# Performance work log

Measured on AMD Instinct MI355X. Metric: run time of the kernel, lower is better.

## Reference

```python
import jax, jax.numpy as jnp
import numpy as np

COUNT = 8  # hardcoded 8x8 patch grid in the original module


def setup_inputs() -> dict:
    key = jax.random.key(0)
    kx, = jax.random.split(key, 1)
    x = jax.random.normal(kx, (8, 64, 512, 512), dtype=jnp.float32)
    gamma = jnp.zeros((1,), dtype=jnp.float32)  # nn.Parameter(torch.zeros(1))
    return {"x": x, "gamma": gamma}


def reference(x, gamma):
    B, C, H, W = x.shape
    s = H // COUNT  # stride; original uses height-derived stride for both dims
    # Extract the 8x8 grid of patches without loops:
    # (B,C,H,W) -> (B,C,cnt,s,cnt,s) -> (B,cnt,cnt,C,s,s) -> (B,P,C,s*s)
    p = x.reshape(B, C, COUNT, s, COUNT, s)
    p = p.transpose(0, 2, 4, 1, 3, 5).reshape(B, COUNT * COUNT, C, s * s)
    # channel-channel energy per patch: [B,P,C,C]
    energy = jnp.einsum('bpci,bpdi->bpcd', p, p)
    # DANet trick: max - energy, then softmax over last dim
    energy_new = jnp.max(energy, axis=-1, keepdims=True) - energy
    attention = jax.nn.softmax(energy_new, axis=-1)
    out = jnp.einsum('bpcd,bpdi->bpci', attention, p)
    # reassemble spatial map
    out = out.reshape(B, COUNT, COUNT, C, s, s)
    out = out.transpose(0, 3, 1, 4, 2, 5).reshape(B, C, H, W)
    # NOTE: in the torch code y = x is an alias and x is overwritten in-place,
    # so the final result is gamma * attended + attended.
    return gamma[0] * out + out
```

## Files before the change

### kernel.cpp

```cpp
#include <hip/hip_runtime.h>


#define NW  512
#define HWs 262144

typedef __attribute__((ext_vector_type(4)))  __bf16 bf4;
typedef __attribute__((ext_vector_type(8)))  __bf16 bf8;
typedef __attribute__((ext_vector_type(16))) float  f32x16;

#define MFMA __builtin_amdgcn_mfma_f32_32x32x16_bf16
#define F4E(v,j) ((j)==0?(v).x:(j)==1?(v).y:(j)==2?(v).z:(v).w)

__device__ __forceinline__ void bar_lgkm() {
  asm volatile("s_waitcnt lgkmcnt(0)" ::: "memory");
  __builtin_amdgcn_s_barrier();
}

extern "C" __global__ __launch_bounds__(512)
void k1_gram(const float* __restrict__ x, float* __restrict__ ep,
             __bf16* __restrict__ wsHi) {
  __shared__ char lds[66560];
  char* sHi = lds;
  char* sLo = lds + 32768;
  float* S_lds = (float*)lds;

  const int T   = threadIdx.x;
  const int wv8 = T >> 6;
  const int l   = T & 63;
  const int l31 = l & 31;
  const int hh  = l >> 5;

  const int bid = blockIdx.x;
  const int wh = bid & 1;
  const int hq = (bid >> 1) & 3;
  const int pr = (bid >> 3) & 7;
  const int b  = bid >> 6;

  const int pl = wv8 & 3;
  const int ct = wv8 >> 2;
  const int pc = wh * 4 + pl;
  const int pat  = b * 64 + pr * 8 + pc;
  const int row0 = pr * 64 + hq * 16;

  const float* xb = x + (size_t)b * 64 * HWs + (size_t)row0 * NW + wh * 256 + l * 4;

  f32x16 G0, G1, S0, S1;
#pragma unroll
  for (int i = 0; i < 16; ++i) { G0[i]=0.f; G1[i]=0.f; S0[i]=0.f; S1[i]=0.f; }

  float4 rA[8], rB[8];
#pragma unroll
  for (int j = 0; j < 8; ++j)
    rA[j] = *(const float4*)(xb + (size_t)(wv8 * 8 + j) * HWs);

  for (int r = 0; r < 16; ++r) {
    if (r + 1 < 16) {
#pragma unroll
      for (int j = 0; j < 8; ++j)
        rB[j] = *(const float4*)(xb + (size_t)(wv8 * 8 + j) * HWs + (size_t)(r + 1) * NW);
    }
    bf4 hA[8];
#pragma unroll
    for (int j = 0; j < 8; ++j) {
      const int c = wv8 * 8 + j;
      const float4 v = rA[j];
      bf4 h, lo;
      h[0]=(__bf16)v.x; h[1]=(__bf16)v.y; h[2]=(__bf16)v.z; h[3]=(__bf16)v.w;
      lo[0]=(__bf16)(v.x-(float)h[0]); lo[1]=(__bf16)(v.y-(float)h[1]);
      lo[2]=(__bf16)(v.z-(float)h[2]); lo[3]=(__bf16)(v.w-(float)h[3]);
      hA[j] = h;
      const int off = c * 512 + ((l * 8) ^ ((c & 31) << 4));
      *(bf4*)(sHi + off) = h;
      *(bf4*)(sLo + off) = lo;
    }
#pragma unroll
    for (int k2 = 0; k2 < 4; ++k2) {
      bf8 pk;
#pragma unroll
      for (int jj = 0; jj < 8; ++jj) pk[jj] = hA[jj][k2];
      const int wloc256 = l * 4 + k2;
      const int pl_w = wloc256 >> 6;
      const int w_loc = wloc256 & 63;
      const int pat_w = b * 64 + pr * 8 + wh * 4 + pl_w;
      const int i = (hq * 16 + r) * 64 + w_loc;
      *(bf8*)((char*)wsHi + (size_t)pat_w * 524288 + (size_t)i * 128 + wv8 * 16) = pk;
    }
    bar_lgkm();
#pragma unroll
    for (int ks = 0; ks < 4; ++ks) {
      const int kb = pl * 128 + ks * 32 + hh * 16;
      const int ca = ct * 32 + l31;
      const bf8 a   = *(const bf8*)(sHi + ca * 512 + (kb ^ ((ca & 31) << 4)));
      const bf8 bh0 = *(const bf8*)(sHi + l31 * 512 + (kb ^ ((l31 & 31) << 4)));
      const bf8 bh1 = *(const bf8*)(sHi + (32 + l31) * 512 + (kb ^ (((32 + l31) & 31) << 4)));
      const bf8 bl0 = *(const bf8*)(sLo + l31 * 512 + (kb ^ ((l31 & 31) << 4)));
      const bf8 bl1 = *(const bf8*)(sLo + (32 + l31) * 512 + (kb ^ (((32 + l31) & 31) << 4)));
      G0 = MFMA(a, bh0, G0, 0, 0, 0);
      G1 = MFMA(a, bh1, G1, 0, 0, 0);
      S0 = MFMA(a, bl0, S0, 0, 0, 0);
      S1 = MFMA(a, bl1, S1, 0, 0, 0);
    }
    bar_lgkm();
#pragma unroll
    for (int e = 0; e < 8; ++e) rA[e] = rB[e];
  }

#pragma unroll
  for (int i = 0; i < 16; ++i) {
    const int cr = ct * 32 + (i & 3) + ((i >> 2) << 3) + (hh << 2);
    S_lds[pl * 4160 + cr * 65 + l31]      = S0[i];
    S_lds[pl * 4160 + cr * 65 + 32 + l31] = S1[i];
  }
  bar_lgkm();
  float* epb = ep + ((size_t)(pat * 4 + hq) << 12);
#pragma unroll
  for (int i = 0; i < 16; ++i) {
    const int cr = ct * 32 + (i & 3) + ((i >> 2) << 3) + (hh << 2);
    epb[cr * 64 + l31]      = G0[i] + S0[i] + S_lds[pl * 4160 + l31 * 65 + cr];
    epb[cr * 64 + 32 + l31] = G1[i] + S1[i] + S_lds[pl * 4160 + (32 + l31) * 65 + cr];
  }
}

extern "C" __global__ __launch_bounds__(256)
void k2_softmax(const float* __restrict__ ep, const float* __restrict__ g,
                __bf16* __restrict__ attn) {
  const int pat = blockIdx.x;
  const int w4 = threadIdx.x >> 6, l = threadIdx.x & 63;
  const float gs = 1.0f + g[0];
  const float* e0 = ep + ((size_t)(pat * 4) << 12);
#pragma unroll 1
  for (int cc = 0; cc < 16; ++cc) {
    const int c = w4 * 16 + cc;
    const int o = c * 64 + l;
    const float e = e0[o] + e0[4096 + o] + e0[8192 + o] + e0[12288 + o];
    float mn = e;
#pragma unroll
    for (int off = 32; off; off >>= 1) mn = fminf(mn, __shfl_xor(mn, off));
    const float w = __expf(mn - e);
    float s = w;
#pragma unroll
    for (int off = 32; off; off >>= 1) s += __shfl_xor(s, off);
    attn[(size_t)pat * 4096 + o] = (__bf16)(gs * w / s);
  }
}

extern "C" __global__ __launch_bounds__(512)
void k3_pv(const __bf16* __restrict__ wsHi, const __bf16* __restrict__ attn,
           float* __restrict__ out) {
  __shared__ char lds[65536];
  const int T   = threadIdx.x;
  const int wv8 = T >> 6;
  const int l   = T & 63;
  const int l31 = l & 31;
  const int hh  = l >> 5;

  const int bid = blockIdx.x;
  const int hq = bid & 3;
  const int pr = (bid >> 2) & 7;
  const int b  = bid >> 5;

  const int ii  = T >> 1;
  const int haf = T & 1;

  float4 rS[4], rT[4];
  {
    const size_t src0 = (size_t)(b * 64 + pr * 8) * 524288 + (size_t)(hq * 1024) * 128;
#pragma unroll
    for (int q = 0; q < 4; ++q)
      rS[q] = *(const float4*)((const char*)wsHi + src0 + (size_t)ii * 128 + haf * 64 + q * 16);
  }

  for (int p = 0; p < 8; ++p) {
    const int pat = b * 64 + pr * 8 + p;
    bf8 af[2][4];
#pragma unroll
    for (int mt = 0; mt < 2; ++mt)
#pragma unroll
      for (int ks = 0; ks < 4; ++ks)
        af[mt][ks] = *(const bf8*)(attn + (size_t)pat * 4096 +
                                   (mt * 32 + l31) * 64 + ks * 16 + hh * 8);

    for (int cc = 0; cc < 4; ++cc) {
      const int s = p * 4 + cc;
      char* buf = lds + (s & 1) * 32768;
#pragma unroll
      for (int q = 0; q < 4; ++q) {
        const int off = ii * 128 + (((haf * 64 + q * 16)) ^ ((ii & 7) << 4));
        *(float4*)(buf + off) = rS[q];
      }
      if (s + 1 < 32) {
        const int pn = (s + 1) >> 2, cn = (s + 1) & 3;
        const size_t src = (size_t)(b * 64 + pr * 8 + pn) * 524288 +
                           (size_t)(hq * 1024 + cn * 256) * 128;
#pragma unroll
        for (int q = 0; q < 4; ++q)
          rT[q] = *(const float4*)((const char*)wsHi + src + (size_t)ii * 128 + haf * 64 + q * 16);
      }
      bar_lgkm();

      f32x16 o0, o1;
#pragma unroll
      for (int i = 0; i < 16; ++i) { o0[i] = 0.f; o1[i] = 0.f; }
#pragma unroll
      for (int ks = 0; ks < 4; ++ks) {
        const int irow = wv8 * 32 + l31;
        const bf8 pa = *(const bf8*)(buf + irow * 128 +
                                     (((ks * 32 + hh * 16)) ^ ((irow & 7) << 4)));
        o0 = MFMA(pa, af[0][ks], o0, 0, 0, 0);
        o1 = MFMA(pa, af[1][ks], o1, 0, 0, 0);
      }
      const int i_base = hq * 1024 + cc * 256 + wv8 * 32;
#pragma unroll
      for (int rq = 0; rq < 4; ++rq) {
        const int ig = i_base + rq * 8 + hh * 4;
        const int rl = ig >> 6, wl = ig & 63;
        float* orow = out + (size_t)b * 64 * HWs + (size_t)(pr * 64 + rl) * NW + p * 64 + wl;
        float4 q0; q0.x=o0[rq*4+0]; q0.y=o0[rq*4+1]; q0.z=o0[rq*4+2]; q0.w=o0[rq*4+3];
        *(float4*)(orow + (size_t)l31 * HWs) = q0;
        float4 q1; q1.x=o1[rq*4+0]; q1.y=o1[rq*4+1]; q1.z=o1[rq*4+2]; q1.w=o1[rq*4+3];
        *(float4*)(orow + (size_t)(32 + l31) * HWs) = q1;
      }
      bar_lgkm();
#pragma unroll
      for (int e = 0; e < 4; ++e) rS[e] = rT[e];
    }
  }
}

#define NS1 16
#define NS3 16
__device__ __forceinline__ void fb_load1(const float* g1, int st, float4 (&R)[16]) {
  const float* gp = g1 + (size_t)st * 4 * NW;
#pragma unroll
  for (int rl = 0; rl < 4; ++rl)
#pragma unroll
    for (int j = 0; j < 4; ++j)
      R[rl * 4 + j] = *(const float4*)(gp + (size_t)rl * NW + j * 4);
}
__device__ __forceinline__ void fb_cvtw1(char* wH, char* wL, int q_ld, int swzw,
                                         const float4 (&R)[16]) {
#pragma unroll
  for (int rl = 0; rl < 4; ++rl)
#pragma unroll
    for (int s = 0; s < 2; ++s) {
      const float4 va = R[rl * 4 + s * 2], vb = R[rl * 4 + s * 2 + 1];
      const float f[8] = {va.x, va.y, va.z, va.w, vb.x, vb.y, vb.z, vb.w};
      bf8 h, lo;
#pragma unroll
      for (int e = 0; e < 8; ++e) { h[e] = (__bf16)f[e]; lo[e] = (__bf16)(f[e] - (float)h[e]); }
      const int boff = (rl * 128 + q_ld * 32 + s * 16) ^ swzw;
      *(bf8*)(wH + boff) = h;
      *(bf8*)(wL + boff) = lo;
    }
}
__device__ __forceinline__ void fb_load3(const float* g3, int st, float4 (&R)[16]) {
  const float* gp = g3 + (size_t)st * 4 * NW;
#pragma unroll
  for (int cc = 0; cc < 4; ++cc)
#pragma unroll
    for (int j = 0; j < 4; ++j)
      R[cc * 4 + j] = *(const float4*)(gp + (size_t)cc * HWs + j * 4);
}
__device__ __forceinline__ void fb_cvtw3(char* sT, int cg, int iq, const float4 (&R)[16]) {
#pragma unroll
  for (int w = 0; w < 16; ++w) {
    bf4 q;
#pragma unroll
    for (int cc = 0; cc < 4; ++cc) q[cc] = (__bf16)F4E(R[cc * 4 + (w >> 2)], w & 3);
    const int iloc = iq * 16 + w;
    const int sw = ((iloc & 15) ^ ((iloc >> 4) & 7)) << 4;
    const int boff = (iloc & 127) * 256 + ((((iloc >> 7) << 7) + cg * 8) ^ sw);
    *(bf4*)(sT + boff) = q;
  }
}
extern "C" __global__ __launch_bounds__(256, 2)
void spectralAgg_fallback(const float* __restrict__ x, const float* __restrict__ g,
                          float* __restrict__ out) {
  __shared__ char lds[73728];
  char* sH = lds;
  char* sL = lds + 32768;
  char* sA = lds + 65536;
  const int t = threadIdx.x, wv = t >> 6, l = t & 63, l31 = l & 31, hh = l >> 5;
  const int wg = blockIdx.x, b = wg >> 6, pp = wg & 63, pr = pp >> 3, pcq = pp & 7;
  const size_t pbase = (size_t)b*64*HWs + (size_t)(pr*64)*NW + (size_t)(pcq*64);
  const float* xp = x + pbase;
  float* op = out + pbase;
  const int c_ld = t >> 2, q_ld = t & 3;
  const float* g1 = xp + (size_t)c_ld * HWs + q_ld * 16;
  char* wH = sH + c_ld * 512;
  char* wL = sL + c_ld * 512;
  const int swzw = (c_ld & 31) << 4;
  const int ct = wv >> 1, dt = wv & 1;
  const char* pA  = sH + (size_t)(ct*32+l31)*512;
  const char* pBh = sH + (size_t)(dt*32+l31)*512;
  const char* pBl = sL + (size_t)(dt*32+l31)*512;
  const int swzr = l31 << 4;
  f32x16 accG, accS;
#pragma unroll
  for (int i = 0; i < 16; ++i) { accG[i] = 0.f; accS[i] = 0.f; }
  float4 ra[16], rb[16];
  fb_load1(g1, 0, ra);
  for (int st = 0; st < NS1; ++st) {
    fb_load1(g1, (st + 1 < NS1) ? st + 1 : st, rb);
    fb_cvtw1(wH, wL, q_ld, swzw, ra);
    bar_lgkm();
#pragma unroll
    for (int k0 = 0; k0 < 16; ++k0) {
      const int off = (k0 * 32 + hh * 16) ^ swzr;
      const bf8 a  = *(const bf8*)(pA + off);
      const bf8 bh = *(const bf8*)(pBh + off);
      const bf8 bl = *(const bf8*)(pBl + off);
      accG = MFMA(a, bh, accG, 0, 0, 0);
      accS = MFMA(a, bl, accS, 0, 0, 0);
    }
    bar_lgkm();
#pragma unroll
    for (int e = 0; e < 16; ++e) ra[e] = rb[e];
  }
  float* S_lds = (float*)sL;
  float* E_lds = (float*)sH;
#pragma unroll
  for (int i = 0; i < 16; ++i) {
    const int cr = ct*32 + (i&3) + ((i>>2)<<3) + (hh<<2);
    S_lds[cr*64 + dt*32 + l31] = accS[i];
  }
  bar_lgkm();
#pragma unroll
  for (int i = 0; i < 16; ++i) {
    const int cr = ct*32 + (i&3) + ((i>>2)<<3) + (hh<<2);
    const int d = dt*32 + l31;
    E_lds[cr*64 + d] = accG[i] + accS[i] + S_lds[d*64 + cr];
  }
  bar_lgkm();
  const int cg = t >> 4, iq = t & 15;
  const float* g3 = xp + (size_t)(cg*4)*HWs + (size_t)(iq>>2)*NW + (iq&3)*16;
  fb_load3(g3, 0, ra);
  const float gs = 1.0f + g[0];
#pragma unroll 1
  for (int rr = 0; rr < 16; ++rr) {
    const int c = wv*16 + rr;
    const float e = E_lds[c*64 + l];
    float mn = e;
#pragma unroll
    for (int o = 32; o; o >>= 1) mn = fminf(mn, __shfl_xor(mn, o));
    const float w = __expf(mn - e);
    float s = w;
#pragma unroll
    for (int o = 32; o; o >>= 1) s += __shfl_xor(s, o);
    *(__bf16*)(sA + c*128 + ((l*2) ^ ((c&7)<<4))) = (__bf16)(gs * w / s);
  }
  bar_lgkm();
  bf8 bfr[2][4];
#pragma unroll
  for (int c2 = 0; c2 < 2; ++c2)
#pragma unroll
    for (int k0 = 0; k0 < 4; ++k0)
      bfr[c2][k0] = *(const bf8*)(sA + (size_t)(c2*32+l31)*128 +
                                  ((k0*32 + hh*16) ^ ((l31&7)<<4)));
  for (int st = 0; st < NS3; ++st) {
    fb_load3(g3, (st + 1 < NS3) ? st + 1 : st, rb);
    fb_cvtw3(sH, cg, iq, ra);
    bar_lgkm();
    f32x16 oo0[2], oo1[2];
#pragma unroll
    for (int it = 0; it < 2; ++it)
#pragma unroll
      for (int i = 0; i < 16; ++i) { oo0[it][i] = 0.f; oo1[it][i] = 0.f; }
#pragma unroll
    for (int it = 0; it < 2; ++it) {
      const int i = wv*64 + it*32 + l31;
      const char* base = sH + (size_t)(i & 127) * 256;
      const int hb = (i >> 7) * 128;
      const int sw = ((i & 15) ^ ((i >> 4) & 7)) << 4;
#pragma unroll
      for (int k0 = 0; k0 < 4; ++k0) {
        const bf8 pa = *(const bf8*)(base + ((hb + k0*32 + hh*16) ^ sw));
        oo0[it] = MFMA(pa, bfr[0][k0], oo0[it], 0, 0, 0);
        oo1[it] = MFMA(pa, bfr[1][k0], oo1[it], 0, 0, 0);
      }
    }
#pragma unroll
    for (int it = 0; it < 2; ++it)
#pragma unroll
      for (int rq = 0; rq < 4; ++rq) {
        const int iloc = wv*64 + it*32 + rq*8 + hh*4;
        const int gi = st*256 + iloc;
        float* oprow = op + (size_t)(gi >> 6)*NW + (gi & 63);
        float4 q0; q0.x=oo0[it][rq*4+0]; q0.y=oo0[it][rq*4+1]; q0.z=oo0[it][rq*4+2]; q0.w=oo0[it][rq*4+3];
        *(float4*)(oprow + (size_t)l31*HWs) = q0;
        float4 q1; q1.x=oo1[it][rq*4+0]; q1.y=oo1[it][rq*4+1]; q1.z=oo1[it][rq*4+2]; q1.w=oo1[it][rq*4+3];
        *(float4*)(oprow + (size_t)(32+l31)*HWs) = q1;
      }
    bar_lgkm();
#pragma unroll
    for (int e = 0; e < 16; ++e) ra[e] = rb[e];
  }
}

extern "C" void kernel_launch(void* const* d_in, const int* in_sizes, int n_in,
                              void* d_out, int out_size, void* d_ws, size_t ws_size,
                              hipStream_t stream) {
  const float* x = (const float*)d_in[0];
  const float* g = (const float*)d_in[1];
  float* o = (float*)d_out;
  const size_t epB  = (size_t)512 * 4 * 4096 * 4;
  const size_t aB   = (size_t)512 * 4096 * 2;
  const size_t hiB  = (size_t)512 * 524288;
  if (ws_size >= epB + aB + hiB) {
    float*  ep   = (float*)d_ws;
    __bf16* attn = (__bf16*)((char*)d_ws + epB);
    __bf16* wsHi = (__bf16*)((char*)d_ws + epB + aB);
    k1_gram<<<dim3(512), dim3(512), 0, stream>>>(x, ep, wsHi);
    k2_softmax<<<dim3(512), dim3(256), 0, stream>>>(ep, g, attn);
    k3_pv<<<dim3(256), dim3(512), 0, stream>>>(wsHi, attn, o);
  } else {
    spectralAgg_fallback<<<dim3(512), dim3(256), 0, stream>>>(x, g, o);
  }
}
```

Baseline: 410.8 us.

## Drop bf16 patch workspace; recompute PV operands directly from fp32 input

The gram kernel no longer writes a transposed bf16 copy of the patches to workspace. The PV kernel instead rereads x in fp32, converts it to bf16 and transposes it through LDS per row, using the same 512-block tiling as the gram kernel. It also walks blocks in reverse order, presumably so the early blocks reuse x data the previous kernel left in cache. This removes a 256MB workspace write and its reread, at the cost of reading 512MB of fp32 input again plus extra conversion and per-row barriers.

Measured after the change: 402.6 us. 1.02x faster.

```diff
diff --git a/kernel.cpp b/kernel.cpp
--- a/kernel.cpp
+++ b/kernel.cpp
@@ -16,9 +16,12 @@
   __builtin_amdgcn_s_barrier();
 }
 
+__device__ __forceinline__ int soff(int c, int rb) {
+  return c * 512 + (rb ^ ((c & 31) << 4));
+}
+
 extern "C" __global__ __launch_bounds__(512)
-void k1_gram(const float* __restrict__ x, float* __restrict__ ep,
-             __bf16* __restrict__ wsHi) {
+void k1_gram(const float* __restrict__ x, float* __restrict__ ep) {
   __shared__ char lds[66560];
   char* sHi = lds;
   char* sLo = lds + 32768;
@@ -27,8 +30,7 @@
   const int T   = threadIdx.x;
   const int wv8 = T >> 6;
   const int l   = T & 63;
-  const int l31 = l & 31;
-  const int hh  = l >> 5;
+  const int l31 = l & 31, hh = l >> 5;
 
   const int bid = blockIdx.x;
   const int wh = bid & 1;
@@ -38,8 +40,7 @@
 
   const int pl = wv8 & 3;
   const int ct = wv8 >> 2;
-  const int pc = wh * 4 + pl;
-  const int pat  = b * 64 + pr * 8 + pc;
+  const int pat  = b * 64 + pr * 8 + wh * 4 + pl;
   const int row0 = pr * 64 + hq * 16;
 
   const float* xb = x + (size_t)b * 64 * HWs + (size_t)row0 * NW + wh * 256 + l * 4;
@@ -59,7 +60,6 @@
       for (int j = 0; j < 8; ++j)
         rB[j] = *(const float4*)(xb + (size_t)(wv8 * 8 + j) * HWs + (size_t)(r + 1) * NW);
     }
-    bf4 hA[8];
 #pragma unroll
     for (int j = 0; j < 8; ++j) {
       const int c = wv8 * 8 + j;
@@ -68,33 +68,20 @@
       h[0]=(__bf16)v.x; h[1]=(__bf16)v.y; h[2]=(__bf16)v.z; h[3]=(__bf16)v.w;
       lo[0]=(__bf16)(v.x-(float)h[0]); lo[1]=(__bf16)(v.y-(float)h[1]);
       lo[2]=(__bf16)(v.z-(float)h[2]); lo[3]=(__bf16)(v.w-(float)h[3]);
-      hA[j] = h;
       const int off = c * 512 + ((l * 8) ^ ((c & 31) << 4));
       *(bf4*)(sHi + off) = h;
       *(bf4*)(sLo + off) = lo;
     }
-#pragma unroll
-    for (int k2 = 0; k2 < 4; ++k2) {
-      bf8 pk;
-#pragma unroll
-      for (int jj = 0; jj < 8; ++jj) pk[jj] = hA[jj][k2];
-      const int wloc256 = l * 4 + k2;
-      const int pl_w = wloc256 >> 6;
-      const int w_loc = wloc256 & 63;
-      const int pat_w = b * 64 + pr * 8 + wh * 4 + pl_w;
-      const int i = (hq * 16 + r) * 64 + w_loc;
-      *(bf8*)((char*)wsHi + (size_t)pat_w * 524288 + (size_t)i * 128 + wv8 * 16) = pk;
-    }
     bar_lgkm();
 #pragma unroll
     for (int ks = 0; ks < 4; ++ks) {
-      const int kb = pl * 128 + ks * 32 + hh * 16;
+      const int rb = pl * 128 + ks * 32 + hh * 16;
       const int ca = ct * 32 + l31;
-      const bf8 a   = *(const bf8*)(sHi + ca * 512 + (kb ^ ((ca & 31) << 4)));
-      const bf8 bh0 = *(const bf8*)(sHi + l31 * 512 + (kb ^ ((l31 & 31) << 4)));
-      const bf8 bh1 = *(const bf8*)(sHi + (32 + l31) * 512 + (kb ^ (((32 + l31) & 31) << 4)));
-      const bf8 bl0 = *(const bf8*)(sLo + l31 * 512 + (kb ^ ((l31 & 31) << 4)));
-      const bf8 bl1 = *(const bf8*)(sLo + (32 + l31) * 512 + (kb ^ (((32 + l31) & 31) << 4)));
+      const bf8 a   = *(const bf8*)(sHi + soff(ca, rb));
+      const bf8 bh0 = *(const bf8*)(sHi + soff(l31, rb));
+      const bf8 bh1 = *(const bf8*)(sHi + soff(32 + l31, rb));
+      const bf8 bl0 = *(const bf8*)(sLo + soff(l31, rb));
+      const bf8 bl1 = *(const bf8*)(sLo + soff(32 + l31, rb));
       G0 = MFMA(a, bh0, G0, 0, 0, 0);
       G1 = MFMA(a, bh1, G1, 0, 0, 0);
       S0 = MFMA(a, bl0, S0, 0, 0, 0);
@@ -144,86 +131,79 @@
   }
 }
 
-extern "C" __global__ __launch_bounds__(512)
-void k3_pv(const __bf16* __restrict__ wsHi, const __bf16* __restrict__ attn,
+extern "C" __global__ __launch_bounds__(512, 4)
+void k3_pv(const float* __restrict__ x, const __bf16* __restrict__ attn,
            float* __restrict__ out) {
-  __shared__ char lds[65536];
+  __shared__ char pT[256 * 144];
+
   const int T   = threadIdx.x;
   const int wv8 = T >> 6;
   const int l   = T & 63;
-  const int l31 = l & 31;
-  const int hh  = l >> 5;
-
-  const int bid = blockIdx.x;
-  const int hq = bid & 3;
-  const int pr = (bid >> 2) & 7;
-  const int b  = bid >> 5;
-
-  const int ii  = T >> 1;
-  const int haf = T & 1;
-
-  float4 rS[4], rT[4];
-  {
-    const size_t src0 = (size_t)(b * 64 + pr * 8) * 524288 + (size_t)(hq * 1024) * 128;
-#pragma unroll
-    for (int q = 0; q < 4; ++q)
-      rS[q] = *(const float4*)((const char*)wsHi + src0 + (size_t)ii * 128 + haf * 64 + q * 16);
-  }
-
-  for (int p = 0; p < 8; ++p) {
-    const int pat = b * 64 + pr * 8 + p;
-    bf8 af[2][4];
-#pragma unroll
-    for (int mt = 0; mt < 2; ++mt)
-#pragma unroll
-      for (int ks = 0; ks < 4; ++ks)
-        af[mt][ks] = *(const bf8*)(attn + (size_t)pat * 4096 +
-                                   (mt * 32 + l31) * 64 + ks * 16 + hh * 8);
-
-    for (int cc = 0; cc < 4; ++cc) {
-      const int s = p * 4 + cc;
-      char* buf = lds + (s & 1) * 32768;
-#pragma unroll
-      for (int q = 0; q < 4; ++q) {
-        const int off = ii * 128 + (((haf * 64 + q * 16)) ^ ((ii & 7) << 4));
-        *(float4*)(buf + off) = rS[q];
-      }
-      if (s + 1 < 32) {
-        const int pn = (s + 1) >> 2, cn = (s + 1) & 3;
-        const size_t src = (size_t)(b * 64 + pr * 8 + pn) * 524288 +
-                           (size_t)(hq * 1024 + cn * 256) * 128;
-#pragma unroll
-        for (int q = 0; q < 4; ++q)
-          rT[q] = *(const float4*)((const char*)wsHi + src + (size_t)ii * 128 + haf * 64 + q * 16);
-      }
-      bar_lgkm();
-
-      f32x16 o0, o1;
-#pragma unroll
-      for (int i = 0; i < 16; ++i) { o0[i] = 0.f; o1[i] = 0.f; }
-#pragma unroll
-      for (int ks = 0; ks < 4; ++ks) {
-        const int irow = wv8 * 32 + l31;
-        const bf8 pa = *(const bf8*)(buf + irow * 128 +
-                                     (((ks * 32 + hh * 16)) ^ ((irow & 7) << 4)));
-        o0 = MFMA(pa, af[0][ks], o0, 0, 0, 0);
-        o1 = MFMA(pa, af[1][ks], o1, 0, 0, 0);
-      }
-      const int i_base = hq * 1024 + cc * 256 + wv8 * 32;
-#pragma unroll
-      for (int rq = 0; rq < 4; ++rq) {
-        const int ig = i_base + rq * 8 + hh * 4;
-        const int rl = ig >> 6, wl = ig & 63;
-        float* orow = out + (size_t)b * 64 * HWs + (size_t)(pr * 64 + rl) * NW + p * 64 + wl;
-        float4 q0; q0.x=o0[rq*4+0]; q0.y=o0[rq*4+1]; q0.z=o0[rq*4+2]; q0.w=o0[rq*4+3];
-        *(float4*)(orow + (size_t)l31 * HWs) = q0;
-        float4 q1; q1.x=o1[rq*4+0]; q1.y=o1[rq*4+1]; q1.z=o1[rq*4+2]; q1.w=o1[rq*4+3];
-        *(float4*)(orow + (size_t)(32 + l31) * HWs) = q1;
-      }
-      bar_lgkm();
-#pragma unroll
-      for (int e = 0; e < 4; ++e) rS[e] = rT[e];
-    }
+  const int l31 = l & 31, hh = l >> 5;
+
+  const int bid = 511 - (int)blockIdx.x;
+  const int wh = bid & 1;
+  const int hq = (bid >> 1) & 3;
+  const int pr = (bid >> 3) & 7;
+  const int b  = bid >> 6;
+  const int row0 = pr * 64 + hq * 16;
+
+  const float* xb = x + (size_t)b * 64 * HWs + (size_t)row0 * NW + wh * 256 + l * 4;
+  float* ob = out + (size_t)b * 64 * HWs + (size_t)row0 * NW + wh * 256;
+
+  const int pl = wv8 & 3, ih = wv8 >> 2;
+  const int pat = b * 64 + pr * 8 + wh * 4 + pl;
+
+  bf8 af[2][4];
+#pragma unroll
+  for (int mt = 0; mt < 2; ++mt)
+#pragma unroll
+    for (int ks = 0; ks < 4; ++ks)
+      af[mt][ks] = *(const bf8*)(attn + (size_t)pat * 4096 +
+                                 (mt * 32 + l31) * 64 + ks * 16 + hh * 8);
+
+  float4 rA[8], rB[8];
+#pragma unroll
+  for (int j = 0; j < 8; ++j)
+    rA[j] = *(const float4*)(xb + (size_t)(wv8 * 8 + j) * HWs);
+
+  for (int r = 0; r < 16; ++r) {
+    if (r + 1 < 16) {
+#pragma unroll
+      for (int j = 0; j < 8; ++j)
+        rB[j] = *(const float4*)(xb + (size_t)(wv8 * 8 + j) * HWs + (size_t)(r + 1) * NW);
+    }
+#pragma unroll
+    for (int q = 0; q < 4; ++q) {
+      bf8 v;
+#pragma unroll
+      for (int j = 0; j < 8; ++j) v[j] = (__bf16)F4E(rA[j], q);
+      *(bf8*)(pT + (size_t)(l * 4 + q) * 144 + wv8 * 16) = v;
+    }
+    bar_lgkm();
+
+    f32x16 o0, o1;
+#pragma unroll
+    for (int i = 0; i < 16; ++i) { o0[i] = 0.f; o1[i] = 0.f; }
+    const int wrow = pl * 64 + ih * 32 + l31;
+#pragma unroll
+    for (int ks = 0; ks < 4; ++ks) {
+      const bf8 pa = *(const bf8*)(pT + (size_t)wrow * 144 + ks * 32 + hh * 16);
+      o0 = MFMA(pa, af[0][ks], o0, 0, 0, 0);
+      o1 = MFMA(pa, af[1][ks], o1, 0, 0, 0);
+    }
+#pragma unroll
+    for (int rq = 0; rq < 4; ++rq) {
+      const int w = pl * 64 + ih * 32 + rq * 8 + hh * 4;
+      float* orow = ob + (size_t)r * NW + w;
+      float4 q0; q0.x=o0[rq*4+0]; q0.y=o0[rq*4+1]; q0.z=o0[rq*4+2]; q0.w=o0[rq*4+3];
+      *(float4*)(orow + (size_t)l31 * HWs) = q0;
+      float4 q1; q1.x=o1[rq*4+0]; q1.y=o1[rq*4+1]; q1.z=o1[rq*4+2]; q1.w=o1[rq*4+3];
+      *(float4*)(orow + (size_t)(32 + l31) * HWs) = q1;
+    }
+    bar_lgkm();
+#pragma unroll
+    for (int e = 0; e < 8; ++e) rA[e] = rB[e];
   }
 }
 
@@ -403,16 +383,14 @@
   const float* x = (const float*)d_in[0];
   const float* g = (const float*)d_in[1];
   float* o = (float*)d_out;
-  const size_t epB  = (size_t)512 * 4 * 4096 * 4;
-  const size_t aB   = (size_t)512 * 4096 * 2;
-  const size_t hiB  = (size_t)512 * 524288;
-  if (ws_size >= epB + aB + hiB) {
+  const size_t epB = (size_t)512 * 4 * 4096 * 4;
+  const size_t aB  = (size_t)512 * 4096 * 2;
+  if (ws_size >= epB + aB) {
     float*  ep   = (float*)d_ws;
     __bf16* attn = (__bf16*)((char*)d_ws + epB);
-    __bf16* wsHi = (__bf16*)((char*)d_ws + epB + aB);
-    k1_gram<<<dim3(512), dim3(512), 0, stream>>>(x, ep, wsHi);
+    k1_gram   <<<dim3(512), dim3(512), 0, stream>>>(x, ep);
     k2_softmax<<<dim3(512), dim3(256), 0, stream>>>(ep, g, attn);
-    k3_pv<<<dim3(256), dim3(512), 0, stream>>>(wsHi, attn, o);
+    k3_pv     <<<dim3(512), dim3(512), 0, stream>>>(x, attn, o);
   } else {
     spectralAgg_fallback<<<dim3(512), dim3(256), 0, stream>>>(x, g, o);
   }
```
